# Kernel optimization log

Measured on AMD Instinct MI355X. Metric: run time of the kernel, lower is better.

## Reference

```python
import jax, jax.numpy as jnp
import numpy as np

HIDDEN = 2048
N_HEADS = 16
N_KV_HEADS = 4
HEAD_DIM = HIDDEN // N_HEADS  # 128
FFN = 4096
N_EXPERTS = 8
TOP_K = 2
T = 2048
EPS = 1e-5
ROPE_THETA = 10000.0


def setup_inputs() -> dict:
    key = jax.random.key(0)
    ks = jax.random.split(key, 10)
    s = 0.02
    q_size = N_HEADS * HEAD_DIM
    kv_size = N_KV_HEADS * HEAD_DIM
    return {
        "hidden_states": jax.random.normal(ks[0], (T, HIDDEN), jnp.float32),
        "positions": jnp.arange(T, dtype=jnp.int32),
        "norm1_w": jnp.ones((HIDDEN,), jnp.float32),
        "norm2_w": jnp.ones((HIDDEN,), jnp.float32),
        "wqkv": jax.random.normal(ks[1], (q_size + 2 * kv_size, HIDDEN), jnp.float32) * s,
        "wo": jax.random.normal(ks[2], (HIDDEN, q_size), jnp.float32) * s,
        "gate_w": jax.random.normal(ks[3], (N_EXPERTS, HIDDEN), jnp.float32) * s,
        "w1": jax.random.normal(ks[4], (N_EXPERTS, FFN, HIDDEN), jnp.float32) * s,
        "w2": jax.random.normal(ks[5], (N_EXPERTS, HIDDEN, FFN), jnp.float32) * s,
        "w3": jax.random.normal(ks[6], (N_EXPERTS, FFN, HIDDEN), jnp.float32) * s,
    }


def _rms_norm(x, w):
    var = jnp.mean(x * x, axis=-1, keepdims=True)
    return x * jax.lax.rsqrt(var + EPS) * w


def _rope(x, positions):
    # neox-style rotary: x [T, H, D], split in halves
    half = HEAD_DIM // 2
    inv_freq = 1.0 / (ROPE_THETA ** (jnp.arange(0, half, dtype=jnp.float32) * 2.0 / HEAD_DIM))
    ang = positions.astype(jnp.float32)[:, None] * inv_freq[None, :]  # [T, half]
    cos = jnp.cos(ang)[:, None, :]  # [T, 1, half]
    sin = jnp.sin(ang)[:, None, :]
    x1, x2 = x[..., :half], x[..., half:]
    return jnp.concatenate([x1 * cos - x2 * sin, x2 * cos + x1 * sin], axis=-1)


def reference(hidden_states, positions, norm1_w, norm2_w, wqkv, wo, gate_w, w1, w2, w3):
    q_size = N_HEADS * HEAD_DIM
    kv_size = N_KV_HEADS * HEAD_DIM

    # --- input RMSNorm + attention ---
    residual = hidden_states
    h = _rms_norm(hidden_states, norm1_w)
    qkv = h @ wqkv.T  # [T, q+2kv]
    q = qkv[:, :q_size].reshape(T, N_HEADS, HEAD_DIM)
    k = qkv[:, q_size:q_size + kv_size].reshape(T, N_KV_HEADS, HEAD_DIM)
    v = qkv[:, q_size + kv_size:].reshape(T, N_KV_HEADS, HEAD_DIM)
    q = _rope(q, positions)
    k = _rope(k, positions)
    rep = N_HEADS // N_KV_HEADS
    k = jnp.repeat(k, rep, axis=1)  # [T, H, D]
    v = jnp.repeat(v, rep, axis=1)

    scale = HEAD_DIM ** -0.5
    scores = jnp.einsum('thd,shd->hts', q, k) * scale  # [H, T, T]
    causal = jnp.tril(jnp.ones((T, T), dtype=bool))
    scores = jnp.where(causal[None], scores, jnp.finfo(scores.dtype).min)
    probs = jax.nn.softmax(scores, axis=-1)
    attn = jnp.einsum('hts,shd->thd', probs, v).reshape(T, q_size)
    attn_out = attn @ wo.T

    # --- residual, post-attn RMSNorm ---
    h = attn_out + residual
    residual2 = h
    h = _rms_norm(h, norm2_w)

    # --- MoE: gate -> softmax -> top-k -> renormalize -> SwiGLU experts ---
    logits = h @ gate_w.T  # [T, E]
    routing = jax.nn.softmax(logits.astype(jnp.float32), axis=-1)
    top_vals, top_idx = jax.lax.top_k(routing, TOP_K)  # [T, K]
    top_vals = top_vals / jnp.sum(top_vals, axis=-1, keepdims=True)
    # dense per-token expert weight matrix [T, E] (zero for unselected experts)
    w_full = jnp.zeros((T, N_EXPERTS), jnp.float32).at[
        jnp.arange(T)[:, None], top_idx].add(top_vals)

    h1 = jnp.einsum('td,efd->etf', h, w1)  # [E, T, F]
    h3 = jnp.einsum('td,efd->etf', h, w3)
    g = jax.nn.silu(h1) * h3
    out_e = jnp.einsum('etf,edf->etd', g, w2)  # [E, T, D]
    moe_out = jnp.einsum('etd,te->td', out_e, w_full)

    return moe_out + residual2
```

## Files before the change

kernel.cpp:

```cpp
#include <hip/hip_runtime.h>
#include <math.h>

typedef __fp16 f16;
typedef __fp16 f16x8 __attribute__((ext_vector_type(8)));
typedef __fp16 f16x4 __attribute__((ext_vector_type(4)));
typedef float  f32x4 __attribute__((ext_vector_type(4)));

#define T_SEQ 2048
#define HID   2048
#define NQH   16
#define NKV   4
#define HD    128
#define FFN_D 4096
#define NEXP  8

#define GLDS(gp, lp) __builtin_amdgcn_global_load_lds( \
    (const __attribute__((address_space(1))) void*)(gp), \
    (__attribute__((address_space(3))) void*)(lp), 16, 0, 0)

__device__ __forceinline__ float wredsum(float v){
#pragma unroll
  for (int m = 32; m; m >>= 1) v += __shfl_xor(v, m, 64);
  return v;
}
__device__ __forceinline__ float wredmax(float v){
#pragma unroll
  for (int m = 32; m; m >>= 1) v = fmaxf(v, __shfl_xor(v, m, 64));
  return v;
}

template<bool GATHER_A, bool SCATTER_C, int EPI, int MODE>
__global__ __launch_bounds__(256, 4)
void gemm8(const f16* __restrict__ A, const f16* __restrict__ B,
           const f16* __restrict__ B2,
           void* __restrict__ Cv, void* __restrict__ Cv2,
           int K, int lda, int ldb, int ldc, long sBz,
           const int* __restrict__ grp_off, const int* __restrict__ a_rows,
           const int* __restrict__ c_rows)
{
  __shared__ __align__(16) f16 Lds[2][8192];
  const int bn = blockIdx.x, bm = blockIdx.y, z = blockIdx.z;
  int e = z, half = 0, sel = 0;
  if (MODE == 1) { e = z >> 1; half = z & 1; }
  if (MODE == 2) { e = z & 7;  sel  = z >> 3; }
  const int rowBase  = grp_off[e];
  const int rowCount = grp_off[e + 1] - rowBase;
  if (rowCount <= 0 || bm * 128 >= rowCount) return;
  const f16* Bz = ((MODE == 2 && sel) ? B2 : B) + (long)e * sBz;
  int k0 = 0, kN = K;
  if (MODE == 1) { kN = K >> 1; k0 = half * kN; }
  const int nt = kN >> 5;

  const int tid = threadIdx.x, lane = tid & 63, w = tid >> 6;
  const int wr = w >> 1, wc = w & 1;

  const int srow = tid >> 2;
  const int scol = (((tid & 3) ^ ((tid >> 3) & 3)) << 3);
  int aoff[2], boff[2];
#pragma unroll
  for (int i = 0; i < 2; i++) {
    int r = bm * 128 + i * 64 + srow;
    if (r > rowCount - 1) r = rowCount - 1;
    const int ar = GATHER_A ? a_rows[rowBase + r] : (rowBase + r);
    aoff[i] = ar * lda + scol + k0;
    boff[i] = (bn * 128 + i * 64 + srow) * ldb + scol + k0;
  }

#define STG8(buf, kk) do { f16* _l = &Lds[buf][0]; \
  GLDS(A  + aoff[0] + (kk), _l +        w * 512); \
  GLDS(A  + aoff[1] + (kk), _l + 2048 + w * 512); \
  GLDS(Bz + boff[0] + (kk), _l + 4096 + w * 512); \
  GLDS(Bz + boff[1] + (kk), _l + 6144 + w * 512); } while (0)

  const int fr = lane & 15, fq = lane >> 4;
  const int cp = ((fq ^ ((fr >> 1) & 3)) << 3);
  const int aRow = (wr * 64 + fr) * 32;
  const int bRow = 4096 + (wc * 64 + fr) * 32;

  f32x4 acc[4][4] = {};

  STG8(0, 0);
  if (nt > 1) STG8(1, 32);

  for (int kt = 0; kt < nt; kt++) {
    if (kt + 1 < nt) asm volatile("s_waitcnt vmcnt(4)" ::: "memory");
    else             asm volatile("s_waitcnt vmcnt(0)" ::: "memory");
    __builtin_amdgcn_s_barrier();
    const f16* Lb = &Lds[kt & 1][0];
    f16x8 bf[4], af[4];
#pragma unroll
    for (int n = 0; n < 4; n++) bf[n] = *(const f16x8*)(Lb + bRow + n * 512 + cp);
#pragma unroll
    for (int m = 0; m < 4; m++) af[m] = *(const f16x8*)(Lb + aRow + m * 512 + cp);
    asm volatile("s_waitcnt lgkmcnt(0)" ::: "memory");
    __builtin_amdgcn_sched_barrier(0);
    __builtin_amdgcn_s_barrier();
    if (kt + 2 < nt) STG8(kt & 1, (kt + 2) * 32);
    __builtin_amdgcn_s_setprio(1);
#pragma unroll
    for (int m = 0; m < 4; m++)
#pragma unroll
      for (int n = 0; n < 4; n++)
        acc[m][n] = __builtin_amdgcn_mfma_f32_16x16x32_f16(af[m], bf[n], acc[m][n], 0, 0, 0);
    __builtin_amdgcn_s_setprio(0);
  }
#undef STG8

  float* Cf = (MODE == 1 && half) ? (float*)Cv2 : (float*)Cv;
  f16*   Ch = (MODE == 2 && sel)  ? (f16*)Cv2   : (f16*)Cv;
  const int ccol0 = bn * 128 + wc * 64 + fr;
#pragma unroll
  for (int m = 0; m < 4; m++) {
#pragma unroll
    for (int r = 0; r < 4; r++) {
      const int g = bm * 128 + wr * 64 + m * 16 + fq * 4 + r;
      if (g >= rowCount) continue;
      const long orow = SCATTER_C ? (long)c_rows[rowBase + g] : (long)(rowBase + g);
#pragma unroll
      for (int n = 0; n < 4; n++) {
        const long idx = orow * ldc + (ccol0 + n * 16);
        if (EPI == 3) Ch[idx] = (f16)acc[m][n][r];
        else          Cf[idx] = acc[m][n][r];
      }
    }
  }
}

template<int EPI, int CAUSAL, bool PVK>
__global__ __launch_bounds__(512, 2)
void gemm83(const f16* __restrict__ Ah, const f16* __restrict__ Al,
            const f16* __restrict__ Bh, const f16* __restrict__ Bl,
            void* __restrict__ Cv, int K, int lda, int ldb, int ldc,
            long sAz, long sBz, int bdiv, long sCz,
            const float* __restrict__ resid)
{
  __shared__ __align__(16) f16 Lds[2][32768];
  const int bn = blockIdx.x, bm = blockIdx.y, z = blockIdx.z;
  if (CAUSAL == 1 && bn > bm) return;
  int head = z, chunk = 0;
  if (PVK) { head = z & 7; chunk = z >> 3; }
  int kstart = 0, kend = K;
  if (PVK) {
    const int km = (bm + 1) * 128;
    if (km < kend) kend = km;
    kstart = chunk * 1024;
    if (kstart >= kend) return;
    if (kend > kstart + 1024) kend = kstart + 1024;
  }
  const int nt = (kend - kstart) >> 6;

  const f16* Ahz = Ah + (long)head * sAz;
  const f16* Alz = Al + (long)head * sAz;
  const long zb = (long)(bdiv ? head / bdiv : head) * sBz;
  const f16* Bhz = Bh + zb;
  const f16* Blz = Bl + zb;

  const int tid = threadIdx.x, lane = tid & 63, w = tid >> 6;
  const int wr = w >> 2, wc = w & 3;

  const int srow = w * 8 + (lane >> 3);
  const int scol = (((lane & 7) ^ (lane >> 3)) << 3);
  long ar[2], br[2];
#pragma unroll
  for (int i = 0; i < 2; i++) {
    ar[i] = (long)(bm * 128 + i * 64 + srow) * lda + scol + kstart;
    br[i] = (long)(bn * 128 + i * 64 + srow) * ldb + scol + kstart;
  }

#define STG83(buf, kk) do { f16* _l = &Lds[buf][0]; \
  GLDS(Ahz + ar[0] + (kk), _l +         w * 512); GLDS(Ahz + ar[1] + (kk), _l +  4096 + w * 512); \
  GLDS(Alz + ar[0] + (kk), _l +  8192 + w * 512); GLDS(Alz + ar[1] + (kk), _l + 12288 + w * 512); \
  GLDS(Bhz + br[0] + (kk), _l + 16384 + w * 512); GLDS(Bhz + br[1] + (kk), _l + 20480 + w * 512); \
  GLDS(Blz + br[0] + (kk), _l + 24576 + w * 512); GLDS(Blz + br[1] + (kk), _l + 28672 + w * 512); } while (0)

  const int fr = lane & 15, fq = lane >> 4;
  const int cp0 = ((fq       ^ (fr & 7)) << 3);
  const int cp1 = (((4 | fq) ^ (fr & 7)) << 3);
  const int aRow = (wr * 64 + fr) * 64;
  const int bRow = 16384 + (wc * 32 + fr) * 64;

  f32x4 acc[4][2] = {};

  STG83(0, 0);
  if (nt > 1) STG83(1, 64);

  for (int kt = 0; kt < nt; kt++) {
    if (kt + 1 < nt) asm volatile("s_waitcnt vmcnt(8)" ::: "memory");
    else             asm volatile("s_waitcnt vmcnt(0)" ::: "memory");
    __builtin_amdgcn_s_barrier();
    const f16* Lb = &Lds[kt & 1][0];
#pragma unroll
    for (int ks = 0; ks < 2; ks++) {
      const int cp = ks ? cp1 : cp0;
      f16x8 ah[4], al[4], bh[2], bl[2];
#pragma unroll
      for (int n = 0; n < 2; n++) {
        bh[n] = *(const f16x8*)(Lb + bRow +        n * 1024 + cp);
        bl[n] = *(const f16x8*)(Lb + bRow + 8192 + n * 1024 + cp);
      }
#pragma unroll
      for (int m = 0; m < 4; m++) {
        ah[m] = *(const f16x8*)(Lb + aRow +        m * 1024 + cp);
        al[m] = *(const f16x8*)(Lb + aRow + 8192 + m * 1024 + cp);
      }
      __builtin_amdgcn_s_setprio(1);
#pragma unroll
      for (int m = 0; m < 4; m++)
#pragma unroll
        for (int n = 0; n < 2; n++) {
          acc[m][n] = __builtin_amdgcn_mfma_f32_16x16x32_f16(ah[m], bh[n], acc[m][n], 0, 0, 0);
          acc[m][n] = __builtin_amdgcn_mfma_f32_16x16x32_f16(ah[m], bl[n], acc[m][n], 0, 0, 0);
          acc[m][n] = __builtin_amdgcn_mfma_f32_16x16x32_f16(al[m], bh[n], acc[m][n], 0, 0, 0);
        }
      __builtin_amdgcn_s_setprio(0);
    }
    __builtin_amdgcn_s_barrier();
    if (kt + 2 < nt) STG83(kt & 1, (kt + 2) * 64);
  }
#undef STG83

  float* Cf = (float*)Cv + (long)head * sCz + (PVK ? (long)chunk * T_SEQ * HID : 0);
  const int crow0 = bm * 128 + wr * 64 + fq * 4;
  const int ccol0 = bn * 128 + wc * 32 + fr;
#pragma unroll
  for (int m = 0; m < 4; m++) {
#pragma unroll
    for (int r = 0; r < 4; r++) {
      const long row = crow0 + m * 16 + r;
#pragma unroll
      for (int n = 0; n < 2; n++) {
        const long idx = row * ldc + (ccol0 + n * 16);
        const float v = acc[m][n][r];
        if (EPI == 2) Cf[idx] = v + resid[idx];
        else          Cf[idx] = v;
      }
    }
  }
}

template<bool SPLIT>
__global__ __launch_bounds__(256)
void rmsnorm_k(const float* __restrict__ x, const float* __restrict__ w,
               f16* __restrict__ hi, f16* __restrict__ lo, float* __restrict__ invr_out)
{
  const int t = blockIdx.x, tid = threadIdx.x;
  const float4* xr = (const float4*)(x + (long)t * HID);
  const float4 a = xr[tid * 2], b = xr[tid * 2 + 1];
  float ss = a.x*a.x + a.y*a.y + a.z*a.z + a.w*a.w
           + b.x*b.x + b.y*b.y + b.z*b.z + b.w*b.w;
  ss = wredsum(ss);
  __shared__ float red[4];
  if ((tid & 63) == 0) red[tid >> 6] = ss;
  __syncthreads();
  const float tot  = red[0] + red[1] + red[2] + red[3];
  const float invr = 1.0f / sqrtf(tot * (1.0f / HID) + 1e-5f);
  if (invr_out && tid == 0) invr_out[t] = invr;
  const float4* wr4 = (const float4*)w;
  const float4 wa = wr4[tid * 2], wb = wr4[tid * 2 + 1];
  const float vals[8] = { a.x*wa.x, a.y*wa.y, a.z*wa.z, a.w*wa.w,
                          b.x*wb.x, b.y*wb.y, b.z*wb.z, b.w*wb.w };
  f16x8 hv, lv;
#pragma unroll
  for (int j = 0; j < 8; j++) {
    const float y = vals[j] * invr;
    const f16 h = (f16)y;
    hv[j] = h;
    if (SPLIT) lv[j] = (f16)(y - (float)h);
  }
  const long base = (long)t * HID + tid * 8;
  *(f16x8*)(hi + base) = hv;
  if (SPLIT) *(f16x8*)(lo + base) = lv;
}

__global__ __launch_bounds__(256)
void rope_split_k(const float* __restrict__ qkv, const int* __restrict__ pos,
                  f16* __restrict__ qh, f16* __restrict__ ql,
                  f16* __restrict__ kh, f16* __restrict__ kl,
                  f16* __restrict__ vh, f16* __restrict__ vl)
{
  const int t = blockIdx.x, tid = threadIdx.x;
  __shared__ float invf[64];
  if (tid < 64) {
    const float y = (float)tid * (1.0f / 64.0f);
    invf[tid] = 1.0f / (float)pow(10000.0, (double)y);
  }
  __syncthreads();
  const float p = (float)pos[t];
  const float* row = qkv + (long)t * 3072;

#pragma unroll
  for (int i = 0; i < 4; i++) {
    const int pi = tid + i * 256;
    const int h = pi >> 6, d = pi & 63;
    const float ang = p * invf[d];
    float s, c; sincosf(ang, &s, &c);
    const float x1 = row[h * 128 + d], x2 = row[h * 128 + 64 + d];
    const float o1 = x1 * c - x2 * s;
    const float o2 = x2 * c + x1 * s;
    const long base = ((long)h * T_SEQ + t) * HD;
    { const f16 hh = (f16)o1; qh[base + d]      = hh; ql[base + d]      = (f16)(o1 - (float)hh); }
    { const f16 hh = (f16)o2; qh[base + 64 + d] = hh; ql[base + 64 + d] = (f16)(o2 - (float)hh); }
  }
  {
    const int g = tid >> 6, d = tid & 63;
    const float ang = p * invf[d];
    float s, c; sincosf(ang, &s, &c);
    const float x1 = row[2048 + g * 128 + d], x2 = row[2048 + g * 128 + 64 + d];
    const float o1 = x1 * c - x2 * s;
    const float o2 = x2 * c + x1 * s;
    const long base = ((long)g * T_SEQ + t) * HD;
    { const f16 hh = (f16)o1; kh[base + d]      = hh; kl[base + d]      = (f16)(o1 - (float)hh); }
    { const f16 hh = (f16)o2; kh[base + 64 + d] = hh; kl[base + 64 + d] = (f16)(o2 - (float)hh); }
  }
#pragma unroll
  for (int i = 0; i < 2; i++) {
    const int e = tid + i * 256;
    const int g = e >> 7, d = e & 127;
    const float v = row[2560 + e];
    const long idx = ((long)g * HD + d) * T_SEQ + t;
    const f16 h = (f16)v; vh[idx] = h; vl[idx] = (f16)(v - (float)h);
  }
}

__global__ __launch_bounds__(256)
void softmax_pack(float* __restrict__ S)
{
  const int row  = blockIdx.x * 4 + (threadIdx.x >> 6);
  const int lane = threadIdx.x & 63;
  const int t    = row & (T_SEQ - 1);
  const int nseg = (t >> 8) + 1;
  float* Sr = S + (long)row * T_SEQ;
  float4 v[8];
  const float4* Sr4 = (const float4*)Sr;
#pragma unroll
  for (int i = 0; i < 8; i++) if (i < nseg) v[i] = Sr4[i * 64 + lane];
  const float scale = 0.08838834764831843f;
  float vmax = -3.4e38f;
#pragma unroll
  for (int i = 0; i < 8; i++) {
    if (i >= nseg) continue;
    float* pv = (float*)&v[i];
    const int s0 = (i * 64 + lane) * 4;
#pragma unroll
    for (int j = 0; j < 4; j++) {
      const float xx = (s0 + j <= t) ? pv[j] * scale : -3.4e38f;
      pv[j] = xx;
      vmax = fmaxf(vmax, xx);
    }
  }
  vmax = wredmax(vmax);
  float sum = 0.f;
#pragma unroll
  for (int i = 0; i < 8; i++) {
    if (i >= nseg) continue;
    float* pv = (float*)&v[i];
#pragma unroll
    for (int j = 0; j < 4; j++) {
      const float e = (pv[j] > -3.0e38f) ? __expf(pv[j] - vmax) : 0.f;
      pv[j] = e; sum += e;
    }
  }
  sum = wredsum(sum);
  const float rinv = 1.0f / sum;
  __syncthreads();
  f16* P = (f16*)Sr;
#pragma unroll
  for (int i = 0; i < 8; i++) {
    if (i >= nseg) continue;
    const int s0 = (i * 64 + lane) * 4;
    float* pv = (float*)&v[i];
    f16x4 hv, lv;
#pragma unroll
    for (int j = 0; j < 4; j++) {
      const float pr = pv[j] * rinv;
      const f16 ph = (f16)pr;
      hv[j] = ph; lv[j] = (f16)(pr - (float)ph);
    }
    *(f16x4*)(P + s0)         = hv;
    *(f16x4*)(P + T_SEQ + s0) = lv;
  }
}

__global__ __launch_bounds__(256)
void gate_topk(const float* __restrict__ h2, const float* __restrict__ invr,
               const float* __restrict__ n2w, const float* __restrict__ gw,
               int* __restrict__ top_idx, float* __restrict__ top_w)
{
  const int t = blockIdx.x, tid = threadIdx.x;
  const float r = invr[t];
  const float4* xr = (const float4*)(h2 + (long)t * HID);
  const float4 a = xr[tid * 2], b = xr[tid * 2 + 1];
  const float4* wr4 = (const float4*)n2w;
  const float4 wa = wr4[tid * 2], wb = wr4[tid * 2 + 1];
  const float hn[8] = { a.x*wa.x*r, a.y*wa.y*r, a.z*wa.z*r, a.w*wa.w*r,
                        b.x*wb.x*r, b.y*wb.y*r, b.z*wb.z*r, b.w*wb.w*r };
  float part[8];
#pragma unroll
  for (int e = 0; e < 8; e++) {
    const float4* g4 = (const float4*)(gw + (long)e * HID + tid * 8);
    const float4 ga = g4[0], gb = g4[1];
    part[e] = hn[0]*ga.x + hn[1]*ga.y + hn[2]*ga.z + hn[3]*ga.w
            + hn[4]*gb.x + hn[5]*gb.y + hn[6]*gb.z + hn[7]*gb.w;
  }
#pragma unroll
  for (int e = 0; e < 8; e++) part[e] = wredsum(part[e]);
  __shared__ float red[4][8];
  if ((tid & 63) == 0) {
#pragma unroll
    for (int e = 0; e < 8; e++) red[tid >> 6][e] = part[e];
  }
  __syncthreads();
  if (tid == 0) {
    float lg[8];
#pragma unroll
    for (int e = 0; e < 8; e++) lg[e] = red[0][e] + red[1][e] + red[2][e] + red[3][e];
    int i1 = 0;
    for (int e = 1; e < 8; e++) if (lg[e] > lg[i1]) i1 = e;
    int i2 = -1;
    for (int e = 0; e < 8; e++) { if (e == i1) continue; if (i2 < 0 || lg[e] > lg[i2]) i2 = e; }
    const float q = expf(lg[i2] - lg[i1]);
    top_idx[t * 2] = i1; top_idx[t * 2 + 1] = i2;
    top_w[t * 2]     = 1.0f / (1.0f + q);
    top_w[t * 2 + 1] = q / (1.0f + q);
  }
}

__global__ __launch_bounds__(256)
void route_build(const int* __restrict__ ti, int* __restrict__ goff,
                 int* __restrict__ arows, int* __restrict__ crows)
{
  __shared__ int cnt[8], cur[8], off[9];
  const int tid = threadIdx.x;
  if (tid < 8) { cnt[tid] = 0; cur[tid] = 0; }
  __syncthreads();
  for (int i = tid; i < 2 * T_SEQ; i += 256) atomicAdd(&cnt[ti[i]], 1);
  __syncthreads();
  if (tid == 0) {
    int s = 0;
    for (int e = 0; e < NEXP; e++) { off[e] = s; s += cnt[e]; }
    off[NEXP] = s;
    for (int e = 0; e <= NEXP; e++) goff[e] = off[e];
  }
  __syncthreads();
  for (int i = tid; i < 2 * T_SEQ; i += 256) {
    const int e = ti[i];
    const int p = atomicAdd(&cur[e], 1);
    const int slot = off[e] + p;
    arows[slot] = i >> 1;
    crows[slot] = (i & 1) * T_SEQ + (i >> 1);
  }
}

__global__ __launch_bounds__(256)
void silu_mul_k(const f16* __restrict__ h1, const f16* __restrict__ h3, f16* __restrict__ g)
{
  const long i = ((long)blockIdx.x * 256 + threadIdx.x) * 8;
  const f16x8 a = *(const f16x8*)(h1 + i);
  const f16x8 b = *(const f16x8*)(h3 + i);
  f16x8 o;
#pragma unroll
  for (int j = 0; j < 8; j++) {
    const float xx = (float)a[j];
    const float s = xx / (1.0f + __expf(-xx));
    o[j] = (f16)(s * (float)b[j]);
  }
  *(f16x8*)(g + i) = o;
}

__global__ __launch_bounds__(256)
void split_pair_k(const float* __restrict__ src, f16* __restrict__ hi, f16* __restrict__ lo)
{
  const long i = ((long)blockIdx.x * 256 + threadIdx.x) * 8;
  const float4 a = *(const float4*)(src + i);
  const float4 b = *(const float4*)(src + i + 4);
  const float vals[8] = {a.x,a.y,a.z,a.w,b.x,b.y,b.z,b.w};
  f16x8 hv, lv;
#pragma unroll
  for (int j = 0; j < 8; j++) { const f16 h = (f16)vals[j]; hv[j] = h; lv[j] = (f16)(vals[j] - (float)h); }
  *(f16x8*)(hi + i) = hv;
  *(f16x8*)(lo + i) = lv;
}

__global__ __launch_bounds__(256)
void split_sum_k(const float* __restrict__ c0, const float* __restrict__ c1,
                 f16* __restrict__ hi, f16* __restrict__ lo)
{
  const long i = ((long)blockIdx.x * 256 + threadIdx.x) * 8;
  const int t = (int)(i >> 11);
  const float4 a = *(const float4*)(c0 + i);
  const float4 b = *(const float4*)(c0 + i + 4);
  float4 ca = {0,0,0,0}, cb = {0,0,0,0};
  if (t >= 1024) { ca = *(const float4*)(c1 + i); cb = *(const float4*)(c1 + i + 4); }
  const float vals[8] = {a.x+ca.x, a.y+ca.y, a.z+ca.z, a.w+ca.w,
                         b.x+cb.x, b.y+cb.y, b.z+cb.z, b.w+cb.w};
  f16x8 hv, lv;
#pragma unroll
  for (int j = 0; j < 8; j++) { const f16 h = (f16)vals[j]; hv[j] = h; lv[j] = (f16)(vals[j] - (float)h); }
  *(f16x8*)(hi + i) = hv;
  *(f16x8*)(lo + i) = lv;
}

__global__ __launch_bounds__(256)
void conv_f16_k(const float* __restrict__ src, f16* __restrict__ dst)
{
  const long i = ((long)blockIdx.x * 256 + threadIdx.x) * 8;
  const float4 a = *(const float4*)(src + i);
  const float4 b = *(const float4*)(src + i + 4);
  f16x8 o;
  o[0]=(f16)a.x; o[1]=(f16)a.y; o[2]=(f16)a.z; o[3]=(f16)a.w;
  o[4]=(f16)b.x; o[5]=(f16)b.y; o[6]=(f16)b.z; o[7]=(f16)b.w;
  *(f16x8*)(dst + i) = o;
}

__global__ __launch_bounds__(256)
void combine_k(const float* __restrict__ h2, const float* __restrict__ c0,
               const float* __restrict__ c1, const float* __restrict__ tw,
               float* __restrict__ out)
{
  const long i = ((long)blockIdx.x * 256 + threadIdx.x) * 4;
  const int t = (int)(i >> 11);
  const float w0 = tw[t * 2], w1 = tw[t * 2 + 1];
  const float4 a   = *(const float4*)(h2 + i);
  const float4 p0a = *(const float4*)(c0 + i);
  const float4 p0b = *(const float4*)(c1 + i);
  const float4 p1a = *(const float4*)(c0 + (long)T_SEQ * HID + i);
  const float4 p1b = *(const float4*)(c1 + (long)T_SEQ * HID + i);
  float4 o;
  o.x = a.x + w0 * (p0a.x + p0b.x) + w1 * (p1a.x + p1b.x);
  o.y = a.y + w0 * (p0a.y + p0b.y) + w1 * (p1a.y + p1b.y);
  o.z = a.z + w0 * (p0a.z + p0b.z) + w1 * (p1a.z + p1b.z);
  o.w = a.w + w0 * (p0a.w + p0b.w) + w1 * (p1a.w + p1b.w);
  *(float4*)(out + i) = o;
}

extern "C" void kernel_launch(void* const* d_in, const int* in_sizes, int n_in,
                              void* d_out, int out_size, void* d_ws, size_t ws_size,
                              hipStream_t stream)
{
  const float* x    = (const float*)d_in[0];
  const int*   pos  = (const int*)d_in[1];
  const float* n1w  = (const float*)d_in[2];
  const float* n2w  = (const float*)d_in[3];
  const float* wqkv = (const float*)d_in[4];
  const float* wo   = (const float*)d_in[5];
  const float* gw   = (const float*)d_in[6];
  const float* w1   = (const float*)d_in[7];
  const float* w2   = (const float*)d_in[8];
  const float* w3   = (const float*)d_in[9];
  float* out = (float*)d_out;

  char* base = (char*)d_ws;
  size_t off = 0;
  auto alloc = [&](size_t bytes) -> char* {
    char* r = base + off;
    off += (bytes + 255) & ~(size_t)255;
    return r;
  };
  f16* w1h = (f16*)alloc((size_t)NEXP * FFN_D * HID * 2);
  f16* w3h = (f16*)alloc((size_t)NEXP * FFN_D * HID * 2);
  f16* w2h = (f16*)alloc((size_t)NEXP * FFN_D * HID * 2);
  f16* wqh = (f16*)alloc((size_t)3072 * HID * 2);
  f16* wql = (f16*)alloc((size_t)3072 * HID * 2);
  f16* woh = (f16*)alloc((size_t)HID * HID * 2);
  f16* wol = (f16*)alloc((size_t)HID * HID * 2);
  f16* qh  = (f16*)alloc((size_t)NQH * T_SEQ * HD * 2);
  f16* ql  = (f16*)alloc((size_t)NQH * T_SEQ * HD * 2);
  f16* kh  = (f16*)alloc((size_t)NKV * T_SEQ * HD * 2);
  f16* kl  = (f16*)alloc((size_t)NKV * T_SEQ * HD * 2);
  f16* vh  = (f16*)alloc((size_t)NKV * T_SEQ * HD * 2);
  f16* vl  = (f16*)alloc((size_t)NKV * T_SEQ * HD * 2);
  float* h2      = (float*)alloc((size_t)T_SEQ * HID * 4);
  f16*   h2n     = (f16*)alloc((size_t)T_SEQ * HID * 2);
  float* contrib = (float*)alloc((size_t)2 * T_SEQ * HID * 4);
  float* invr2 = (float*)alloc(T_SEQ * 4);
  int*   tidx  = (int*)alloc(T_SEQ * 2 * 4);
  float* twt   = (float*)alloc(T_SEQ * 2 * 4);
  int*   counts = (int*)alloc(256);
  int*   goff   = (int*)alloc(256);
  int*   arows  = (int*)alloc(2 * T_SEQ * 4);
  int*   crows  = (int*)alloc(2 * T_SEQ * 4);
  (void)counts;
  char* uA = alloc((size_t)T_SEQ * 3072 * 4);
  float* qkvf = (float*)uA;
  char* uB = alloc((size_t)T_SEQ * HID * 2);
  f16* hh = (f16*)uB; f16* ahh = (f16*)uB;
  char* uC = alloc((size_t)T_SEQ * HID * 2);
  f16* hl = (f16*)uC; f16* ahl = (f16*)uC;
  char* uS = alloc((size_t)8 * T_SEQ * T_SEQ * 4);
  float* Sbuf = (float*)uS;
  f16* h1b = (f16*)uS;
  f16* h3b = (f16*)(uS + (size_t)2 * T_SEQ * FFN_D * 2);
  f16* gb  = (f16*)(uS + (size_t)4 * T_SEQ * FFN_D * 2);
  float* contribH = (float*)(uS + (size_t)6 * T_SEQ * FFN_D * 2);

  if (off > ws_size) return;

  conv_f16_k<<<(NEXP * FFN_D * HID) / (256 * 8), 256, 0, stream>>>(w1, w1h);
  conv_f16_k<<<(NEXP * FFN_D * HID) / (256 * 8), 256, 0, stream>>>(w3, w3h);
  conv_f16_k<<<(NEXP * FFN_D * HID) / (256 * 8), 256, 0, stream>>>(w2, w2h);
  split_pair_k<<<(3072 * HID) / (256 * 8), 256, 0, stream>>>(wqkv, wqh, wql);
  split_pair_k<<<(HID * HID) / (256 * 8), 256, 0, stream>>>(wo, woh, wol);

  rmsnorm_k<true><<<T_SEQ, 256, 0, stream>>>(x, n1w, hh, hl, nullptr);
  gemm83<0,0,false><<<dim3(3072/128, T_SEQ/128, 1), 512, 0, stream>>>(
      hh, hl, wqh, wql, qkvf, HID, HID, HID, 3072, 0, 0, 0, 0, nullptr);
  rope_split_k<<<T_SEQ, 256, 0, stream>>>(qkvf, pos, qh, ql, kh, kl, vh, vl);

  for (int grp = 0; grp < 2; grp++) {
    const f16* qh_g = qh + (size_t)grp * 8 * T_SEQ * HD;
    const f16* ql_g = ql + (size_t)grp * 8 * T_SEQ * HD;
    const f16* kh_g = kh + (size_t)grp * 2 * T_SEQ * HD;
    const f16* kl_g = kl + (size_t)grp * 2 * T_SEQ * HD;
    const f16* vh_g = vh + (size_t)grp * 2 * HD * T_SEQ;
    const f16* vl_g = vl + (size_t)grp * 2 * HD * T_SEQ;
    float* attn_g = contrib + (size_t)grp * 8 * HD;
    gemm83<0,1,false><<<dim3(T_SEQ/128, T_SEQ/128, 8), 512, 0, stream>>>(
        qh_g, ql_g, kh_g, kl_g, Sbuf, HD, HD, HD, T_SEQ,
        (long)T_SEQ * HD, (long)T_SEQ * HD, 4, (long)T_SEQ * T_SEQ, nullptr);
    softmax_pack<<<8 * T_SEQ / 4, 256, 0, stream>>>(Sbuf);
    gemm83<0,0,true><<<dim3(1, T_SEQ/128, 16), 512, 0, stream>>>(
        (const f16*)Sbuf, (const f16*)Sbuf + T_SEQ, vh_g, vl_g, attn_g,
        T_SEQ, 2 * T_SEQ, T_SEQ, HID,
        (long)T_SEQ * 2 * T_SEQ, (long)HD * T_SEQ, 4, HD, nullptr);
  }

  split_sum_k<<<(T_SEQ * HID) / (256 * 8), 256, 0, stream>>>(contrib, contrib + (size_t)T_SEQ * HID, ahh, ahl);
  gemm83<2,0,false><<<dim3(HID/128, T_SEQ/128, 1), 512, 0, stream>>>(
      ahh, ahl, woh, wol, h2, HID, HID, HID, HID, 0, 0, 0, 0, x);

  rmsnorm_k<false><<<T_SEQ, 256, 0, stream>>>(h2, n2w, h2n, nullptr, invr2);
  gate_topk<<<T_SEQ, 256, 0, stream>>>(h2, invr2, n2w, gw, tidx, twt);
  route_build<<<1, 256, 0, stream>>>(tidx, goff, arows, crows);

  gemm8<true,false,3,2><<<dim3(FFN_D/128, 16, 2 * NEXP), 256, 0, stream>>>(
      h2n, w1h, w3h, h1b, h3b, HID, HID, HID, FFN_D, (long)FFN_D * HID, goff, arows, nullptr);
  silu_mul_k<<<(2 * T_SEQ * FFN_D) / (256 * 8), 256, 0, stream>>>(h1b, h3b, gb);
  gemm8<false,true,0,1><<<dim3(HID/128, 16, 2 * NEXP), 256, 0, stream>>>(
      gb, w2h, nullptr, contrib, contribH, FFN_D, FFN_D, FFN_D, HID, (long)HID * FFN_D, goff, nullptr, crows);
  combine_k<<<(T_SEQ * HID) / (256 * 4), 256, 0, stream>>>(h2, contrib, contribH, twt, out);
}
```

Measured before the change: 998.3 us.

## Fuse w1/w3 expert GEMMs with SiLU epilogue and fold routing weights into down-proj

Adds a dual-B grouped GEMM that computes the gate and up projections together from one shared A tile in LDS and applies SiLU*mul in the epilogue. This removes the separate silu_mul kernel and the h1/h3 intermediate round trips. The down projection now scales by the routing weight and stores f16 partials, so combine reads half the bytes. The cost is two accumulator sets per thread, which raises register pressure and drops occupancy to 2 blocks per CU. The extra f16 rounding of the partials also costs some precision.

```diff
diff --git a/kernel.cpp b/kernel.cpp
--- a/kernel.cpp
+++ b/kernel.cpp
@@ -29,24 +29,120 @@
   return v;
 }
 
+template<bool GATHER_A>
+__global__ __launch_bounds__(256, 2)
+void gemm_ffn(const f16* __restrict__ A, const f16* __restrict__ B1,
+              const f16* __restrict__ B3, f16* __restrict__ G,
+              int K, int lda, int ldb, int ldg, long sBz,
+              const int* __restrict__ grp_off, const int* __restrict__ a_rows)
+{
+  __shared__ __align__(16) f16 Lds[2][12288];
+  const int bn = blockIdx.x, bm = blockIdx.y, e = blockIdx.z;
+  const int rowBase  = grp_off[e];
+  const int rowCount = grp_off[e + 1] - rowBase;
+  if (rowCount <= 0 || bm * 128 >= rowCount) return;
+  const f16* B1z = B1 + (long)e * sBz;
+  const f16* B3z = B3 + (long)e * sBz;
+  const int nt = K >> 5;
+
+  const int tid = threadIdx.x, lane = tid & 63, w = tid >> 6;
+  const int wr = w >> 1, wc = w & 1;
+
+  const int srow = tid >> 2;
+  const int scol = (((tid & 3) ^ ((tid >> 3) & 3)) << 3);
+  int aoff[2], boff[2];
+#pragma unroll
+  for (int i = 0; i < 2; i++) {
+    int r = bm * 128 + i * 64 + srow;
+    if (r > rowCount - 1) r = rowCount - 1;
+    const int ar = GATHER_A ? a_rows[rowBase + r] : (rowBase + r);
+    aoff[i] = ar * lda + scol;
+    boff[i] = (bn * 128 + i * 64 + srow) * ldb + scol;
+  }
+
+#define STGF(buf, kk) do { f16* _l = &Lds[buf][0]; \
+  GLDS(A   + aoff[0] + (kk), _l +         w * 512); \
+  GLDS(A   + aoff[1] + (kk), _l +  2048 + w * 512); \
+  GLDS(B1z + boff[0] + (kk), _l +  4096 + w * 512); \
+  GLDS(B1z + boff[1] + (kk), _l +  6144 + w * 512); \
+  GLDS(B3z + boff[0] + (kk), _l +  8192 + w * 512); \
+  GLDS(B3z + boff[1] + (kk), _l + 10240 + w * 512); } while (0)
+
+  const int fr = lane & 15, fq = lane >> 4;
+  const int cp = ((fq ^ ((fr >> 1) & 3)) << 3);
+  const int aRow  = (wr * 64 + fr) * 32;
+  const int b1Row = 4096 + (wc * 64 + fr) * 32;
+  const int b3Row = 8192 + (wc * 64 + fr) * 32;
+
+  f32x4 acc1[4][4] = {};
+  f32x4 acc3[4][4] = {};
+
+  STGF(0, 0);
+  if (nt > 1) STGF(1, 32);
+
+  for (int kt = 0; kt < nt; kt++) {
+    if (kt + 1 < nt) asm volatile("s_waitcnt vmcnt(6)" ::: "memory");
+    else             asm volatile("s_waitcnt vmcnt(0)" ::: "memory");
+    __builtin_amdgcn_s_barrier();
+    const f16* Lb = &Lds[kt & 1][0];
+    f16x8 af[4], b1f[4], b3f[4];
+#pragma unroll
+    for (int m = 0; m < 4; m++) af[m]  = *(const f16x8*)(Lb + aRow  + m * 512 + cp);
+#pragma unroll
+    for (int n = 0; n < 4; n++) b1f[n] = *(const f16x8*)(Lb + b1Row + n * 512 + cp);
+#pragma unroll
+    for (int n = 0; n < 4; n++) b3f[n] = *(const f16x8*)(Lb + b3Row + n * 512 + cp);
+    asm volatile("s_waitcnt lgkmcnt(0)" ::: "memory");
+    __builtin_amdgcn_sched_barrier(0);
+    __builtin_amdgcn_s_barrier();
+    if (kt + 2 < nt) STGF(kt & 1, (kt + 2) * 32);
+    __builtin_amdgcn_s_setprio(1);
+#pragma unroll
+    for (int m = 0; m < 4; m++)
+#pragma unroll
+      for (int n = 0; n < 4; n++) {
+        acc1[m][n] = __builtin_amdgcn_mfma_f32_16x16x32_f16(af[m], b1f[n], acc1[m][n], 0, 0, 0);
+        acc3[m][n] = __builtin_amdgcn_mfma_f32_16x16x32_f16(af[m], b3f[n], acc3[m][n], 0, 0, 0);
+      }
+    __builtin_amdgcn_s_setprio(0);
+  }
+#undef STGF
+
+  const int ccol0 = bn * 128 + wc * 64 + fr;
+#pragma unroll
+  for (int m = 0; m < 4; m++) {
+#pragma unroll
+    for (int r = 0; r < 4; r++) {
+      const int g = bm * 128 + wr * 64 + m * 16 + fq * 4 + r;
+      if (g >= rowCount) continue;
+      const long orow = rowBase + g;
+#pragma unroll
+      for (int n = 0; n < 4; n++) {
+        const float h1 = acc1[m][n][r];
+        const float h3 = acc3[m][n][r];
+        const float s  = h1 / (1.0f + __expf(-h1));
+        G[orow * ldg + (ccol0 + n * 16)] = (f16)(s * h3);
+      }
+    }
+  }
+}
+
 template<bool GATHER_A, bool SCATTER_C, int EPI, int MODE>
 __global__ __launch_bounds__(256, 4)
 void gemm8(const f16* __restrict__ A, const f16* __restrict__ B,
-           const f16* __restrict__ B2,
            void* __restrict__ Cv, void* __restrict__ Cv2,
            int K, int lda, int ldb, int ldc, long sBz,
            const int* __restrict__ grp_off, const int* __restrict__ a_rows,
-           const int* __restrict__ c_rows)
+           const int* __restrict__ c_rows, const float* __restrict__ tw)
 {
   __shared__ __align__(16) f16 Lds[2][8192];
   const int bn = blockIdx.x, bm = blockIdx.y, z = blockIdx.z;
-  int e = z, half = 0, sel = 0;
+  int e = z, half = 0;
   if (MODE == 1) { e = z >> 1; half = z & 1; }
-  if (MODE == 2) { e = z & 7;  sel  = z >> 3; }
   const int rowBase  = grp_off[e];
   const int rowCount = grp_off[e + 1] - rowBase;
   if (rowCount <= 0 || bm * 128 >= rowCount) return;
-  const f16* Bz = ((MODE == 2 && sel) ? B2 : B) + (long)e * sBz;
+  const f16* Bz = B + (long)e * sBz;
   int k0 = 0, kN = K;
   if (MODE == 1) { kN = K >> 1; k0 = half * kN; }
   const int nt = kN >> 5;
@@ -107,7 +203,7 @@
 #undef STG8
 
   float* Cf = (MODE == 1 && half) ? (float*)Cv2 : (float*)Cv;
-  f16*   Ch = (MODE == 2 && sel)  ? (f16*)Cv2   : (f16*)Cv;
+  f16*   Ch = (MODE == 1 && half) ? (f16*)Cv2   : (f16*)Cv;
   const int ccol0 = bn * 128 + wc * 64 + fr;
 #pragma unroll
   for (int m = 0; m < 4; m++) {
@@ -119,8 +215,12 @@
 #pragma unroll
       for (int n = 0; n < 4; n++) {
         const long idx = orow * ldc + (ccol0 + n * 16);
-        if (EPI == 3) Ch[idx] = (f16)acc[m][n][r];
-        else          Cf[idx] = acc[m][n][r];
+        if (EPI == 4) {
+          const int t = (int)(orow & (T_SEQ - 1)), kk = (int)(orow >> 11);
+          Ch[idx] = (f16)(tw[t * 2 + kk] * acc[m][n][r]);
+        }
+        else if (EPI == 3) Ch[idx] = (f16)acc[m][n][r];
+        else               Cf[idx] = acc[m][n][r];
       }
     }
   }
@@ -452,22 +552,6 @@
 }
 
 __global__ __launch_bounds__(256)
-void silu_mul_k(const f16* __restrict__ h1, const f16* __restrict__ h3, f16* __restrict__ g)
-{
-  const long i = ((long)blockIdx.x * 256 + threadIdx.x) * 8;
-  const f16x8 a = *(const f16x8*)(h1 + i);
-  const f16x8 b = *(const f16x8*)(h3 + i);
-  f16x8 o;
-#pragma unroll
-  for (int j = 0; j < 8; j++) {
-    const float xx = (float)a[j];
-    const float s = xx / (1.0f + __expf(-xx));
-    o[j] = (f16)(s * (float)b[j]);
-  }
-  *(f16x8*)(g + i) = o;
-}
-
-__global__ __launch_bounds__(256)
 void split_pair_k(const float* __restrict__ src, f16* __restrict__ hi, f16* __restrict__ lo)
 {
   const long i = ((long)blockIdx.x * 256 + threadIdx.x) * 8;
@@ -513,23 +597,20 @@
 }
 
 __global__ __launch_bounds__(256)
-void combine_k(const float* __restrict__ h2, const float* __restrict__ c0,
-               const float* __restrict__ c1, const float* __restrict__ tw,
-               float* __restrict__ out)
+void combine_k(const float* __restrict__ h2, const f16* __restrict__ c0,
+               const f16* __restrict__ c1, float* __restrict__ out)
 {
   const long i = ((long)blockIdx.x * 256 + threadIdx.x) * 4;
-  const int t = (int)(i >> 11);
-  const float w0 = tw[t * 2], w1 = tw[t * 2 + 1];
-  const float4 a   = *(const float4*)(h2 + i);
-  const float4 p0a = *(const float4*)(c0 + i);
-  const float4 p0b = *(const float4*)(c1 + i);
-  const float4 p1a = *(const float4*)(c0 + (long)T_SEQ * HID + i);
-  const float4 p1b = *(const float4*)(c1 + (long)T_SEQ * HID + i);
+  const float4 a = *(const float4*)(h2 + i);
+  const f16x4 p0 = *(const f16x4*)(c0 + i);
+  const f16x4 p1 = *(const f16x4*)(c1 + i);
+  const f16x4 q0 = *(const f16x4*)(c0 + (long)T_SEQ * HID + i);
+  const f16x4 q1 = *(const f16x4*)(c1 + (long)T_SEQ * HID + i);
   float4 o;
-  o.x = a.x + w0 * (p0a.x + p0b.x) + w1 * (p1a.x + p1b.x);
-  o.y = a.y + w0 * (p0a.y + p0b.y) + w1 * (p1a.y + p1b.y);
-  o.z = a.z + w0 * (p0a.z + p0b.z) + w1 * (p1a.z + p1b.z);
-  o.w = a.w + w0 * (p0a.w + p0b.w) + w1 * (p1a.w + p1b.w);
+  o.x = a.x + (float)p0[0] + (float)p1[0] + (float)q0[0] + (float)q1[0];
+  o.y = a.y + (float)p0[1] + (float)p1[1] + (float)q0[1] + (float)q1[1];
+  o.z = a.z + (float)p0[2] + (float)p1[2] + (float)q0[2] + (float)q1[2];
+  o.w = a.w + (float)p0[3] + (float)p1[3] + (float)q0[3] + (float)q1[3];
   *(float4*)(out + i) = o;
 }
 
@@ -588,10 +669,8 @@
   f16* hl = (f16*)uC; f16* ahl = (f16*)uC;
   char* uS = alloc((size_t)8 * T_SEQ * T_SEQ * 4);
   float* Sbuf = (float*)uS;
-  f16* h1b = (f16*)uS;
-  f16* h3b = (f16*)(uS + (size_t)2 * T_SEQ * FFN_D * 2);
   f16* gb  = (f16*)(uS + (size_t)4 * T_SEQ * FFN_D * 2);
-  float* contribH = (float*)(uS + (size_t)6 * T_SEQ * FFN_D * 2);
+  f16* contribH = (f16*)(uS + (size_t)6 * T_SEQ * FFN_D * 2);
 
   if (off > ws_size) return;
 
@@ -632,10 +711,10 @@
   gate_topk<<<T_SEQ, 256, 0, stream>>>(h2, invr2, n2w, gw, tidx, twt);
   route_build<<<1, 256, 0, stream>>>(tidx, goff, arows, crows);
 
-  gemm8<true,false,3,2><<<dim3(FFN_D/128, 16, 2 * NEXP), 256, 0, stream>>>(
-      h2n, w1h, w3h, h1b, h3b, HID, HID, HID, FFN_D, (long)FFN_D * HID, goff, arows, nullptr);
-  silu_mul_k<<<(2 * T_SEQ * FFN_D) / (256 * 8), 256, 0, stream>>>(h1b, h3b, gb);
-  gemm8<false,true,0,1><<<dim3(HID/128, 16, 2 * NEXP), 256, 0, stream>>>(
-      gb, w2h, nullptr, contrib, contribH, FFN_D, FFN_D, FFN_D, HID, (long)HID * FFN_D, goff, nullptr, crows);
-  combine_k<<<(T_SEQ * HID) / (256 * 4), 256, 0, stream>>>(h2, contrib, contribH, twt, out);
-}
+  gemm_ffn<true><<<dim3(FFN_D/128, 16, NEXP), 256, 0, stream>>>(
+      h2n, w1h, w3h, gb, HID, HID, HID, FFN_D, (long)FFN_D * HID, goff, arows);
+  gemm8<false,true,4,1><<<dim3(HID/128, 16, 2 * NEXP), 256, 0, stream>>>(
+      gb, w2h, contrib, contribH, FFN_D, FFN_D, FFN_D, HID, (long)HID * FFN_D,
+      goff, nullptr, crows, twt);
+  combine_k<<<(T_SEQ * HID) / (256 * 4), 256, 0, stream>>>(h2, (const f16*)contrib, contribH, out);
+}
```

Measured after the change: 936.9 us. 1.07x faster.
